# Kernel tuning notes

Hardware: AMD Instinct MI355X
Metric: run time of the kernel (lower is better)

## Reference

```python
import jax, jax.numpy as jnp
import numpy as np

B, T, NM = 128, 2048, 8  # batch, nSteps, nMaxwell


def setup_inputs() -> dict:
    key = jax.random.key(0)
    k1, k2, k3 = jax.random.split(key, 3)
    S_e = jax.random.normal(k1, (B, T, 3, 3), dtype=jnp.float32)
    # strictly increasing times per batch element
    dt = jax.random.uniform(k2, (B, T), minval=0.01, maxval=0.1, dtype=jnp.float32)
    t = jnp.cumsum(dt, axis=1)
    # [tau_1..tau_nM, g_infy, g_1..g_nM] -> last dim 2*NM + 1
    PronyParams = jax.random.uniform(k3, (B, T, 2 * NM + 1), minval=0.1, maxval=1.0, dtype=jnp.float32)
    return {"S_e": S_e, "t": t, "PronyParams": PronyParams}


def reference(S_e, t, PronyParams):
    """Viscoelastic 2nd Piola-Kirchhoff stress via recursive Prony update.

    S_e:         [B, T, 3, 3] instantaneous elastic stress
    t:           [B, T] time
    PronyParams: [B, T, 2*nM+1] (relaxation times tau then coefficients g)
    Returns (S, S_infy, Q_sum), each [B, T, 3, 3].
    """
    nM = PronyParams.shape[-1] // 2
    tau = PronyParams[..., :nM]                      # [B,T,nM]
    g = PronyParams[..., nM:]                        # [B,T,nM+1]
    g = g / jnp.sum(g, axis=-1, keepdims=True)
    g_infy = g[..., 0:1]                             # [B,T,1]
    g_i = g[..., 1:]                                 # [B,T,nM]

    Bsz = S_e.shape[0]
    # time-major scan inputs
    xs = (
        jnp.swapaxes(t, 0, 1),      # [T,B]
        jnp.swapaxes(S_e, 0, 1),    # [T,B,3,3]
        jnp.swapaxes(tau, 0, 1),    # [T,B,nM]
        jnp.swapaxes(g_i, 0, 1),    # [T,B,nM]
    )
    init = (
        jnp.zeros((Bsz, nM, 3, 3), S_e.dtype),  # Q_0
        -t[:, 1],                                # t_prev (as in original initializer)
        jnp.zeros((Bsz, 3, 3), S_e.dtype),       # S_prev
        tau[:, 0],
        g_i[:, 0],
    )

    def step(carry, x):
        Q_p, t_p, S_p, tau_p, g_p = carry
        t_c, S_c, tau_c, g_c = x
        g_bar = 0.5 * (g_c + g_p)                 # [B,nM]
        tau_bar = 0.5 * (tau_c + tau_p)           # [B,nM]
        dt = (t_c - t_p)[:, None]                 # [B,1]
        e = jnp.exp(-0.5 * dt / tau_bar)          # exp(-dt/(2 tau_bar))
        term1 = (e * e)[..., None, None]          # exp(-dt/tau_bar), [B,nM,1,1]
        term2 = (e * g_bar)[..., None, None]      # [B,nM,1,1]
        dS = (S_c - S_p)[:, None]                 # [B,1,3,3]
        Q = term1 * Q_p + term2 * dS              # [B,nM,3,3]
        return (Q, t_c, S_c, tau_c, g_c), Q

    _, Qs = jax.lax.scan(step, init, xs)          # [T,B,nM,3,3]
    Q_sum = jnp.swapaxes(jnp.sum(Qs, axis=2), 0, 1)  # [B,T,3,3]
    S_infy = g_infy[..., None] * S_e              # [B,T,1,1] * [B,T,3,3]
    S = S_infy + Q_sum
    return (S, S_infy, Q_sum)
```

## Files before the change

kernel.cpp:

```cpp
#include <hip/hip_runtime.h>

#define T_LEN 2048
#define NMODE 8
#define NPP   17

template <int L, int G>
__global__ __launch_bounds__(256, 8)
void fused(const float* __restrict__ Se,
           const float* __restrict__ tt,
           const float* __restrict__ pp,
           float* __restrict__ out,
           float* __restrict__ spine,
           unsigned* __restrict__ flags,
           unsigned* __restrict__ ticket,
           int B) {
    constexpr int NSTEP = G * L;
    constexpr int TILES = T_LEN / NSTEP;
    constexpr int RW    = NSTEP + 1;
    constexpr int NT    = 256;
    constexpr int SROW  = NSTEP + 4;
    constexpr int QT_SZ = 9 * SROW;
    constexpr int CA_K  = L * 8 + 4;
    constexpr int AC_K  = L * 16 + 4;
    constexpr int O_AC  = QT_SZ + G * CA_K;
    constexpr int OV_ZREL = 0;
    constexpr int OV_PP   = G * 72;
    constexpr int OV_Z    = OV_PP + G * 8;
    constexpr int OV_R    = OV_Z + G * 72;
    constexpr int OV_P    = OV_R + G * 72;
    static_assert(OV_P + G * 8 <= G * AC_K, "overlay fits in AC region");
    constexpr int O_INV = O_AC + G * AC_K;
    constexpr int O_GI  = O_INV + RW;
    constexpr int TOTAL = O_GI + RW;
    static_assert(TOTAL * 4 <= 20480, "LDS must allow 8 blocks/CU");
    static_assert(L == 16, "epilogue uses t>>4 / t&15");

    __shared__ __align__(16) float sm[TOTAL];
    float* s_qT   = sm;
    float* s_ca   = sm + QT_SZ;
    float* s_AC   = sm + O_AC;
    float* s_Zrel = sm + O_AC + OV_ZREL;
    float* s_Pp   = sm + O_AC + OV_PP;
    float* s_Z    = sm + O_AC + OV_Z;
    float* s_R    = sm + O_AC + OV_R;
    float* s_P    = sm + O_AC + OV_P;
    float* s_inv  = sm + O_INV;
    float* s_gi   = sm + O_GI;

    const int tid = threadIdx.x;

    __shared__ unsigned s_vid;
    if (tid == 0) {
        unsigned stripe = (unsigned)blockIdx.x & 7u;
        unsigned idx = atomicAdd(&ticket[stripe], 1u);
        s_vid = idx * 8u + stripe;
    }
    __syncthreads();
    const int vid  = (int)(s_vid % (unsigned)(B * TILES));
    const int tile = vid / B;
    const int b    = vid % B;

    const int base = tile * NSTEP;
    const int off  = (base == 0) ? 0 : 1;
    const int r0   = (base == 0) ? 0 : base - 1;

    const float* ppb = pp + ((size_t)b * T_LEN + r0) * NPP;
    const float* ttb = tt + (size_t)b * T_LEN + r0;

    for (int i = tid; i < RW; i += NT) {
        const float* gp = ppb + i * NPP + 8;
        float gs = 0.f;
        #pragma unroll
        for (int k = 0; k < 9; ++k) gs += gp[k];
        float iv = __builtin_amdgcn_rcpf(gs);
        s_inv[i] = iv;
        s_gi[i]  = gp[0] * iv;
    }
    __syncthreads();

    for (int i = tid; i < NSTEP * 8; i += NT) {
        int m  = i & 7;
        int ts = i >> 3;
        int rc = ts + off;
        bool first = (base == 0) && (ts == 0);
        int rp = first ? rc : rc - 1;
        float tau_c = ppb[rc * NPP + m];
        float tau_p = ppb[rp * NPP + m];
        float gqh_c = 0.5f * ppb[rc * NPP + 9 + m] * s_inv[rc];
        float gqh_p = 0.5f * ppb[rp * NPP + 9 + m] * s_inv[rp];
        float t_c = ttb[rc];
        float t_p = first ? -ttb[1] : ttb[rp];
        float ee  = __expf((t_p - t_c) * __builtin_amdgcn_rcpf(tau_c + tau_p));
        int kk = ts / L, sl = ts % L;
        s_AC[kk * AC_K + sl * 16 + m]     = ee * ee;
        s_AC[kk * AC_K + sl * 16 + 8 + m] = ee * (gqh_c + gqh_p);
    }
    __syncthreads();

    const size_t nOut = (size_t)B * T_LEN * 9;
    float* o0 = out + ((size_t)b * T_LEN + base) * 9;
    float* o1 = o0 + nOut;
    float* o2 = o0 + 2 * nOut;
    const float4* sv4 = (const float4*)(Se + ((size_t)b * T_LEN + base) * 9);

    float Q[8] = {0,0,0,0,0,0,0,0};
    float cumA_c = 1.f;
    if (tid < 72) {
        const int k = tid / 9;
        const int e = tid - k * 9;
        const float* Sg = Se + (size_t)b * T_LEN * 9 + e;
        const int gbase = base + k * L;

        float dS[L];
        {
            float prev = (base == 0 && k == 0) ? 0.f
                                               : Sg[(size_t)(gbase - 1) * 9];
            #pragma unroll
            for (int s = 0; s < L; ++s) {
                float cur = Sg[(size_t)(gbase + s) * 9];
                dS[s] = cur - prev;
                prev = cur;
            }
        }

        const float4* acp = (const float4*)(s_AC + k * AC_K);
        #pragma unroll
        for (int s = 0; s < L; ++s) {
            float4 a0 = acp[4*s], a1 = acp[4*s+1];
            float4 c0v = acp[4*s+2], c1v = acp[4*s+3];
            float d = dS[s];
            Q[0] = a0.x*Q[0] + c0v.x*d;  Q[1] = a0.y*Q[1] + c0v.y*d;
            Q[2] = a0.z*Q[2] + c0v.z*d;  Q[3] = a0.w*Q[3] + c0v.w*d;
            Q[4] = a1.x*Q[4] + c1v.x*d;  Q[5] = a1.y*Q[5] + c1v.y*d;
            Q[6] = a1.z*Q[6] + c1v.z*d;  Q[7] = a1.w*Q[7] + c1v.w*d;
            float qs = ((Q[0]+Q[1])+(Q[2]+Q[3])) + ((Q[4]+Q[5])+(Q[6]+Q[7]));
            s_qT[e * SROW + (k * L + s)] = qs;
        }
    } else if (tid < 192) {
        for (int i4 = tid - 72; i4 < NSTEP * 9 / 4; i4 += 120) {
            float4 sv = sv4[i4];
            int i = i4 * 4;
            float f0 = s_gi[(i    ) / 9 + off] * sv.x;
            float f1 = s_gi[(i + 1) / 9 + off] * sv.y;
            float f2 = s_gi[(i + 2) / 9 + off] * sv.z;
            float f3 = s_gi[(i + 3) / 9 + off] * sv.w;
            ((float4*)o1)[i4] = make_float4(f0, f1, f2, f3);
        }
    } else {
        const int u = tid - 192;
        const int k = u >> 3;
        const int m = u & 7;
        #pragma unroll
        for (int s = 0; s < L; ++s) {
            cumA_c *= s_AC[k * AC_K + s * 16 + m];
            s_ca[k * CA_K + s * 8 + m] = cumA_c;
        }
    }
    __syncthreads();

    if (tid < 72) {
        float4* r4 = (float4*)(s_R + 8 * tid);
        r4[0] = make_float4(Q[0], Q[1], Q[2], Q[3]);
        r4[1] = make_float4(Q[4], Q[5], Q[6], Q[7]);
    } else if (tid >= 192) {
        s_P[tid - 192] = cumA_c;
    }
    __syncthreads();

    if (tid < 72) {
        const int e = tid >> 3;
        const int m = tid & 7;
        float z = 0.f, pprod = 1.f;
        #pragma unroll
        for (int k = 0; k < G; ++k) {
            s_Zrel[k * 72 + tid] = z;
            if (e == 0) s_Pp[k * 8 + m] = pprod;
            float Pk = s_P[k * 8 + m];
            z = Pk * z + s_R[k * 72 + tid];
            pprod *= Pk;
        }
        if (tile != TILES - 1) {
            float* sp = spine + ((size_t)b * TILES + tile) * 80;
            __hip_atomic_store(sp + 8 + tid, z, __ATOMIC_RELAXED,
                               __HIP_MEMORY_SCOPE_AGENT);
            if (e == 0)
                __hip_atomic_store(sp + m, pprod, __ATOMIC_RELAXED,
                                   __HIP_MEMORY_SCOPE_AGENT);
        }
    }
    if (tile != TILES - 1)
        asm volatile("s_waitcnt vmcnt(0)" ::: "memory");
    __syncthreads();

    if (tile != TILES - 1 && tid == 0)
        __hip_atomic_store(&flags[(size_t)b * TILES + tile], 1u,
                           __ATOMIC_RELAXED, __HIP_MEMORY_SCOPE_AGENT);

    if (tile > 0 && tid < 64) {
        bool done = (tid >= tile);
        while (!__all(done)) {
            if (!done) {
                unsigned f = __hip_atomic_load(
                    &flags[(size_t)b * TILES + tid],
                    __ATOMIC_RELAXED, __HIP_MEMORY_SCOPE_AGENT);
                done = (f != 0u);
                if (!done) __builtin_amdgcn_s_sleep(1);
            }
        }
    }
    __syncthreads();

    float zin = 0.f;
    if (tid < 72 && tile > 0) {
        const int m = tid & 7;
        const float* spb = spine + (size_t)b * TILES * 80;
        float Pv[TILES - 1], Rv[TILES - 1];
        #pragma unroll
        for (int j = 0; j < TILES - 1; ++j) {
            if (j < tile) {
                Pv[j] = __hip_atomic_load(spb + j * 80 + m,
                                          __ATOMIC_RELAXED,
                                          __HIP_MEMORY_SCOPE_AGENT);
                Rv[j] = __hip_atomic_load(spb + j * 80 + 8 + tid,
                                          __ATOMIC_RELAXED,
                                          __HIP_MEMORY_SCOPE_AGENT);
            }
        }
        #pragma unroll
        for (int j = 0; j < TILES - 1; ++j)
            if (j < tile) zin = Pv[j] * zin + Rv[j];
    }

    if (tid < 72) {
        const int m = tid & 7;
        #pragma unroll
        for (int k = 0; k < G; ++k)
            s_Z[k * 72 + tid] = s_Pp[k * 8 + m] * zin + s_Zrel[k * 72 + tid];
    }
    __syncthreads();

    for (int i4 = tid; i4 < NSTEP * 9 / 4; i4 += NT) {
        float4 sv = sv4[i4];
        const float svc[4] = {sv.x, sv.y, sv.z, sv.w};
        int i = i4 * 4;
        float q[4], f[4];
        #pragma unroll
        for (int j = 0; j < 4; ++j) {
            int idx = i + j;
            int t = idx / 9, e = idx - t * 9;
            int rc = t + off;
            int k = t >> 4, s = t & 15;
            const float4* ca4 = (const float4*)(s_ca + k * CA_K + s * 8);
            const float4* z4  = (const float4*)(s_Z + k * 72 + e * 8);
            float4 cA = ca4[0], cB = ca4[1];
            float4 zA = z4[0],  zB = z4[1];
            float cr = ((cA.x*zA.x + cA.y*zA.y) + (cA.z*zA.z + cA.w*zA.w))
                     + ((cB.x*zB.x + cB.y*zB.y) + (cB.z*zB.z + cB.w*zB.w));
            q[j] = s_qT[e * SROW + t] + cr;
            f[j] = s_gi[rc] * svc[j];
        }
        ((float4*)o2)[i4] = make_float4(q[0], q[1], q[2], q[3]);
        ((float4*)o0)[i4] = make_float4(f[0]+q[0], f[1]+q[1],
                                        f[2]+q[2], f[3]+q[3]);
    }
}

extern "C" void kernel_launch(void* const* d_in, const int* in_sizes, int n_in,
                              void* d_out, int out_size, void* d_ws, size_t ws_size,
                              hipStream_t stream) {
    const float* Se = (const float*)d_in[0];
    const float* tt = (const float*)d_in[1];
    const float* pp = (const float*)d_in[2];
    float* out = (float*)d_out;

    int B = in_sizes[1] / T_LEN;

    constexpr int L = 16;
    constexpr int G = 8;
    constexpr int NSTEP = G * L;
    constexpr int TILES = T_LEN / NSTEP;

    unsigned* ticket = (unsigned*)d_ws;
    unsigned* flags  = ticket + 8;
    size_t ctl_bytes = (size_t)(8 + B * TILES) * sizeof(unsigned);
    size_t spine_off = (ctl_bytes + 15) & ~(size_t)15;
    float* spine = (float*)((char*)d_ws + spine_off);

    hipMemsetAsync(d_ws, 0, ctl_bytes, stream);

    fused<L, G><<<B * TILES, dim3(256), 0, stream>>>(
        Se, tt, pp, out, spine, flags, ticket, B);
}
```

Baseline: 118.8 us.

## Replace decoupled-lookback spine with two-kernel scan and separate fixup pass

```diff
diff --git a/kernel.cpp b/kernel.cpp
--- a/kernel.cpp
+++ b/kernel.cpp
@@ -6,13 +6,12 @@
 
 template <int L, int G>
 __global__ __launch_bounds__(256, 8)
-void fused(const float* __restrict__ Se,
+void scanK(const float* __restrict__ Se,
            const float* __restrict__ tt,
            const float* __restrict__ pp,
            float* __restrict__ out,
-           float* __restrict__ spine,
-           unsigned* __restrict__ flags,
-           unsigned* __restrict__ ticket,
+           float* __restrict__ caT,
+           float* __restrict__ agg,
            int B) {
     constexpr int NSTEP = G * L;
     constexpr int TILES = T_LEN / NSTEP;
@@ -25,8 +24,7 @@
     constexpr int O_AC  = QT_SZ + G * CA_K;
     constexpr int OV_ZREL = 0;
     constexpr int OV_PP   = G * 72;
-    constexpr int OV_Z    = OV_PP + G * 8;
-    constexpr int OV_R    = OV_Z + G * 72;
+    constexpr int OV_R    = OV_PP + G * 8;
     constexpr int OV_P    = OV_R + G * 72;
     static_assert(OV_P + G * 8 <= G * AC_K, "overlay fits in AC region");
     constexpr int O_INV = O_AC + G * AC_K;
@@ -41,24 +39,14 @@
     float* s_AC   = sm + O_AC;
     float* s_Zrel = sm + O_AC + OV_ZREL;
     float* s_Pp   = sm + O_AC + OV_PP;
-    float* s_Z    = sm + O_AC + OV_Z;
     float* s_R    = sm + O_AC + OV_R;
     float* s_P    = sm + O_AC + OV_P;
     float* s_inv  = sm + O_INV;
     float* s_gi   = sm + O_GI;
 
     const int tid = threadIdx.x;
-
-    __shared__ unsigned s_vid;
-    if (tid == 0) {
-        unsigned stripe = (unsigned)blockIdx.x & 7u;
-        unsigned idx = atomicAdd(&ticket[stripe], 1u);
-        s_vid = idx * 8u + stripe;
-    }
-    __syncthreads();
-    const int vid  = (int)(s_vid % (unsigned)(B * TILES));
-    const int tile = vid / B;
-    const int b    = vid % B;
+    const int b    = blockIdx.x / TILES;
+    const int tile = blockIdx.x % TILES;
 
     const int base = tile * NSTEP;
     const int off  = (base == 0) ? 0 : 1;
@@ -98,9 +86,8 @@
     __syncthreads();
 
     const size_t nOut = (size_t)B * T_LEN * 9;
-    float* o0 = out + ((size_t)b * T_LEN + base) * 9;
-    float* o1 = o0 + nOut;
-    float* o2 = o0 + 2 * nOut;
+    float* o1 = out + nOut + ((size_t)b * T_LEN + base) * 9;
+    float* o2 = out + 2 * nOut + ((size_t)b * T_LEN + base) * 9;
     const float4* sv4 = (const float4*)(Se + ((size_t)b * T_LEN + base) * 9);
 
     float Q[8] = {0,0,0,0,0,0,0,0};
@@ -180,88 +167,116 @@
             pprod *= Pk;
         }
         if (tile != TILES - 1) {
-            float* sp = spine + ((size_t)b * TILES + tile) * 80;
-            __hip_atomic_store(sp + 8 + tid, z, __ATOMIC_RELAXED,
-                               __HIP_MEMORY_SCOPE_AGENT);
-            if (e == 0)
-                __hip_atomic_store(sp + m, pprod, __ATOMIC_RELAXED,
-                                   __HIP_MEMORY_SCOPE_AGENT);
-        }
-    }
-    if (tile != TILES - 1)
-        asm volatile("s_waitcnt vmcnt(0)" ::: "memory");
-    __syncthreads();
-
-    if (tile != TILES - 1 && tid == 0)
-        __hip_atomic_store(&flags[(size_t)b * TILES + tile], 1u,
-                           __ATOMIC_RELAXED, __HIP_MEMORY_SCOPE_AGENT);
-
-    if (tile > 0 && tid < 64) {
-        bool done = (tid >= tile);
-        while (!__all(done)) {
-            if (!done) {
-                unsigned f = __hip_atomic_load(
-                    &flags[(size_t)b * TILES + tid],
-                    __ATOMIC_RELAXED, __HIP_MEMORY_SCOPE_AGENT);
-                done = (f != 0u);
-                if (!done) __builtin_amdgcn_s_sleep(1);
-            }
-        }
-    }
-    __syncthreads();
-
-    float zin = 0.f;
-    if (tid < 72 && tile > 0) {
-        const int m = tid & 7;
-        const float* spb = spine + (size_t)b * TILES * 80;
-        float Pv[TILES - 1], Rv[TILES - 1];
-        #pragma unroll
-        for (int j = 0; j < TILES - 1; ++j) {
-            if (j < tile) {
-                Pv[j] = __hip_atomic_load(spb + j * 80 + m,
-                                          __ATOMIC_RELAXED,
-                                          __HIP_MEMORY_SCOPE_AGENT);
-                Rv[j] = __hip_atomic_load(spb + j * 80 + 8 + tid,
-                                          __ATOMIC_RELAXED,
-                                          __HIP_MEMORY_SCOPE_AGENT);
-            }
-        }
-        #pragma unroll
-        for (int j = 0; j < TILES - 1; ++j)
-            if (j < tile) zin = Pv[j] * zin + Rv[j];
-    }
-
-    if (tid < 72) {
-        const int m = tid & 7;
-        #pragma unroll
-        for (int k = 0; k < G; ++k)
-            s_Z[k * 72 + tid] = s_Pp[k * 8 + m] * zin + s_Zrel[k * 72 + tid];
-    }
-    __syncthreads();
+            float* ap = agg + ((size_t)b * TILES + tile) * 80;
+            ap[8 + tid] = z;
+            if (e == 0) ap[m] = pprod;
+        }
+    }
+    __syncthreads();
+
+    {
+        int k = tid >> 5;
+        int s = (tid >> 1) & 15;
+        int h = tid & 1;
+        float4 cv = *(const float4*)(s_ca + k * CA_K + s * 8 + h * 4);
+        float4 pv = *(const float4*)(s_Pp + k * 8 + h * 4);
+        float4 ov = make_float4(cv.x*pv.x, cv.y*pv.y, cv.z*pv.z, cv.w*pv.w);
+        *(float4*)(caT + (((size_t)b * T_LEN + base) + k * L + s) * 8 + h * 4)
+            = ov;
+    }
 
     for (int i4 = tid; i4 < NSTEP * 9 / 4; i4 += NT) {
-        float4 sv = sv4[i4];
-        const float svc[4] = {sv.x, sv.y, sv.z, sv.w};
         int i = i4 * 4;
-        float q[4], f[4];
+        float q[4];
         #pragma unroll
         for (int j = 0; j < 4; ++j) {
             int idx = i + j;
             int t = idx / 9, e = idx - t * 9;
-            int rc = t + off;
             int k = t >> 4, s = t & 15;
             const float4* ca4 = (const float4*)(s_ca + k * CA_K + s * 8);
-            const float4* z4  = (const float4*)(s_Z + k * 72 + e * 8);
+            const float4* z4  = (const float4*)(s_Zrel + k * 72 + e * 8);
             float4 cA = ca4[0], cB = ca4[1];
             float4 zA = z4[0],  zB = z4[1];
             float cr = ((cA.x*zA.x + cA.y*zA.y) + (cA.z*zA.z + cA.w*zA.w))
                      + ((cB.x*zB.x + cB.y*zB.y) + (cB.z*zB.z + cB.w*zB.w));
             q[j] = s_qT[e * SROW + t] + cr;
-            f[j] = s_gi[rc] * svc[j];
         }
         ((float4*)o2)[i4] = make_float4(q[0], q[1], q[2], q[3]);
-        ((float4*)o0)[i4] = make_float4(f[0]+q[0], f[1]+q[1],
-                                        f[2]+q[2], f[3]+q[3]);
+    }
+}
+
+template <int L, int G>
+__global__ __launch_bounds__(256, 8)
+void finishK(float* __restrict__ out,
+             const float* __restrict__ caT,
+             const float* __restrict__ agg,
+             int B) {
+    constexpr int NSTEP = G * L;
+    constexpr int TILES = T_LEN / NSTEP;
+    constexpr int NT    = 256;
+
+    __shared__ __align__(16) float s_Z[80];
+    __shared__ __align__(16) float s_ca[NSTEP * 8];
+
+    const int tid  = threadIdx.x;
+    const int b    = blockIdx.x / TILES;
+    const int tile = blockIdx.x % TILES;
+    const int base = tile * NSTEP;
+
+    {
+        const float4* c4 = (const float4*)(caT + ((size_t)b * T_LEN + base) * 8);
+        for (int i = tid; i < NSTEP * 8 / 4; i += NT)
+            ((float4*)s_ca)[i] = c4[i];
+    }
+
+    if (tid < 72) {
+        const int m = tid & 7;
+        float zin = 0.f;
+        if (tile > 0) {
+            const float* ab = agg + (size_t)b * TILES * 80;
+            float Pv[TILES - 1], Rv[TILES - 1];
+            #pragma unroll
+            for (int j = 0; j < TILES - 1; ++j) {
+                if (j < tile) {
+                    Pv[j] = ab[j * 80 + m];
+                    Rv[j] = ab[j * 80 + 8 + tid];
+                }
+            }
+            #pragma unroll
+            for (int j = 0; j < TILES - 1; ++j)
+                if (j < tile) zin = Pv[j] * zin + Rv[j];
+        }
+        s_Z[tid] = zin;
+    }
+    __syncthreads();
+
+    const size_t nOut = (size_t)B * T_LEN * 9;
+    float* o0 = out + ((size_t)b * T_LEN + base) * 9;
+    const float4* sf4 = (const float4*)(o0 + nOut);
+    float4* s4 = (float4*)o0;
+    float4* q4 = (float4*)(o0 + 2 * nOut);
+
+    for (int i4 = tid; i4 < NSTEP * 9 / 4; i4 += NT) {
+        float4 qv = q4[i4];
+        float4 fv = sf4[i4];
+        int i = i4 * 4;
+        float corr[4];
+        #pragma unroll
+        for (int j = 0; j < 4; ++j) {
+            int idx = i + j;
+            int t = idx / 9, e = idx - t * 9;
+            const float4* ca4 = (const float4*)(s_ca + t * 8);
+            const float4* z4  = (const float4*)(s_Z + e * 8);
+            float4 cA = ca4[0], cB = ca4[1];
+            float4 zA = z4[0],  zB = z4[1];
+            corr[j] = ((cA.x*zA.x + cA.y*zA.y) + (cA.z*zA.z + cA.w*zA.w))
+                    + ((cB.x*zB.x + cB.y*zB.y) + (cB.z*zB.z + cB.w*zB.w));
+        }
+        float4 qn = make_float4(qv.x + corr[0], qv.y + corr[1],
+                                qv.z + corr[2], qv.w + corr[3]);
+        q4[i4] = qn;
+        s4[i4] = make_float4(fv.x + qn.x, fv.y + qn.y,
+                             fv.z + qn.z, fv.w + qn.w);
     }
 }
 
@@ -280,14 +295,11 @@
     constexpr int NSTEP = G * L;
     constexpr int TILES = T_LEN / NSTEP;
 
-    unsigned* ticket = (unsigned*)d_ws;
-    unsigned* flags  = ticket + 8;
-    size_t ctl_bytes = (size_t)(8 + B * TILES) * sizeof(unsigned);
-    size_t spine_off = (ctl_bytes + 15) & ~(size_t)15;
-    float* spine = (float*)((char*)d_ws + spine_off);
-
-    hipMemsetAsync(d_ws, 0, ctl_bytes, stream);
-
-    fused<L, G><<<B * TILES, dim3(256), 0, stream>>>(
-        Se, tt, pp, out, spine, flags, ticket, B);
+    float* caT = (float*)d_ws;
+    float* agg = caT + (size_t)B * T_LEN * 8;
+
+    scanK<L, G><<<B * TILES, dim3(256), 0, stream>>>(
+        Se, tt, pp, out, caT, agg, B);
+    finishK<L, G><<<B * TILES, dim3(256), 0, stream>>>(
+        out, caT, agg, B);
 }
```

Result: faster. 98.73 us (median of 2 runs) (-16.9%).
